# Performance work log

Hardware: AMD Instinct MI355X
Metric: run time of the kernel (lower is better)

Reference implementation:

```python
import jax, jax.numpy as jnp
import numpy as np

B, H, W, C = 16, 64, 64, 256
HEADS, WS, SHIFTS, QD = 8, 8, (0, 4), 512
N = WS * WS
HD = C // HEADS
MLP_H = 4 * C
DEPTH = 2
EPS = 1e-5


def _rel_pos_index():
    coords = np.stack(np.meshgrid(np.arange(WS), np.arange(WS), indexing='ij'))  # [2,ws,ws]
    flat = coords.reshape(2, -1)
    rel = (flat[:, :, None] - flat[:, None, :]).transpose(1, 2, 0)  # [N,N,2]
    rel[..., 0] += WS - 1
    rel[..., 1] += WS - 1
    rel[..., 0] *= 2 * WS - 1
    return jnp.asarray(rel.sum(-1))  # [N,N] int


def _shift_mask(shift):
    img = np.zeros((H, W))
    cnt = 0
    for hs in (slice(0, -WS), slice(-WS, -shift), slice(-shift, None)):
        for ws_ in (slice(0, -WS), slice(-WS, -shift), slice(-shift, None)):
            img[hs, ws_] = cnt
            cnt += 1
    mw = img.reshape(H // WS, WS, W // WS, WS).transpose(0, 2, 1, 3).reshape(-1, N)  # [nW,N]
    am = mw[:, None, :] - mw[:, :, None]
    return jnp.asarray(np.where(am != 0, -100.0, 0.0).astype(np.float32))  # [nW,N,N]


RPI = _rel_pos_index()


def layernorm(x, g, b):
    mu = x.mean(-1, keepdims=True)
    var = ((x - mu) ** 2).mean(-1, keepdims=True)
    return (x - mu) * jax.lax.rsqrt(var + EPS) * g + b


def window_partition(x):  # [B,H,W,C] -> [B*nW, N, C]
    x = x.reshape(B, H // WS, WS, W // WS, WS, C)
    return x.transpose(0, 1, 3, 2, 4, 5).reshape(-1, N, C)


def window_reverse(w):  # [B*nW, N, C] -> [B,H,W,C]
    x = w.reshape(B, H // WS, W // WS, WS, WS, C)
    return x.transpose(0, 1, 3, 2, 4, 5).reshape(B, H, W, C)


def swin_block(x, shift, n1g, n1b, qkvw, qkvb, rpb, pw, pb, n2g, n2b, f1w, f1b, f2w, f2b):
    shortcut = x
    y = layernorm(x, n1g, n1b).reshape(B, H, W, C)
    if shift > 0:
        y = jnp.roll(y, (-shift, -shift), axis=(1, 2))
    xw = window_partition(y)                                      # [B_, N, C]
    qkv = (xw @ qkvw + qkvb).reshape(-1, N, 3, HEADS, HD)
    q, k, v = (qkv[:, :, i].transpose(0, 2, 1, 3) for i in range(3))  # [B_,h,N,hd]
    scores = jnp.einsum('bhnd,bhmd->bhnm', q * (HD ** -0.5), k)
    bias = rpb[RPI].transpose(2, 0, 1)                            # [h,N,N]
    scores = scores + bias[None]
    if shift > 0:
        mask = _shift_mask(shift)                                 # [nW,N,N]
        nW = mask.shape[0]
        scores = scores.reshape(B, nW, HEADS, N, N) + mask[None, :, None]
        scores = scores.reshape(-1, HEADS, N, N)
    attn = jax.nn.softmax(scores, axis=-1)
    out = jnp.einsum('bhnm,bhmd->bhnd', attn, v).transpose(0, 2, 1, 3).reshape(-1, N, C)
    out = out @ pw + pb
    y = window_reverse(out)
    if shift > 0:
        y = jnp.roll(y, (shift, shift), axis=(1, 2))
    x = shortcut + y.reshape(B, H * W, C)
    h = layernorm(x, n2g, n2b)
    h = jax.nn.gelu(h @ f1w + f1b, approximate=False) @ f2w + f2b
    return x + h


def cross_attn(x, cond, cng, cnb, inw, inb, outw, outb):
    xn = layernorm(x, cng, cnb)
    q = xn @ inw[:C].T + inb[:C]
    k = cond @ inw[C:2 * C].T + inb[C:2 * C]
    v = cond @ inw[2 * C:].T + inb[2 * C:]
    Tq, Tk = q.shape[1], k.shape[1]
    q = q.reshape(B, Tq, HEADS, HD).transpose(0, 2, 1, 3) * (HD ** -0.5)
    k = k.reshape(B, Tk, HEADS, HD).transpose(0, 2, 1, 3)
    v = v.reshape(B, Tk, HEADS, HD).transpose(0, 2, 1, 3)
    a = jax.nn.softmax(jnp.einsum('bhqd,bhkd->bhqk', q, k), axis=-1)
    o = jnp.einsum('bhqk,bhkd->bhqd', a, v).transpose(0, 2, 1, 3).reshape(B, Tq, C)
    return x + o @ outw.T + outb


def setup_inputs() -> dict:
    key = jax.random.key(0)
    ks = iter(jax.random.split(key, 40))
    s = 0.02
    d = {
        'x': jax.random.normal(next(ks), (B, H * W, C), jnp.float32),
        'emb': jax.random.normal(next(ks), (B, 1, QD), jnp.float32),
        'qenc_w': jax.random.normal(next(ks), (QD, C)) * s,
        'qenc_b': jnp.zeros((C,)),
        'n1_g': jnp.ones((DEPTH, C)), 'n1_b': jnp.zeros((DEPTH, C)),
        'qkv_w': jax.random.normal(next(ks), (DEPTH, C, 3 * C)) * s,
        'qkv_b': jnp.zeros((DEPTH, 3 * C)),
        'rpb': jax.random.normal(next(ks), (DEPTH, (2 * WS - 1) ** 2, HEADS)) * s,
        'proj_w': jax.random.normal(next(ks), (DEPTH, C, C)) * s,
        'proj_b': jnp.zeros((DEPTH, C)),
        'n2_g': jnp.ones((DEPTH, C)), 'n2_b': jnp.zeros((DEPTH, C)),
        'fc1_w': jax.random.normal(next(ks), (DEPTH, C, MLP_H)) * s,
        'fc1_b': jnp.zeros((DEPTH, MLP_H)),
        'fc2_w': jax.random.normal(next(ks), (DEPTH, MLP_H, C)) * s,
        'fc2_b': jnp.zeros((DEPTH, C)),
        'cn_g': jnp.ones((DEPTH, C)), 'cn_b': jnp.zeros((DEPTH, C)),
        'ca_in_w': jax.random.normal(next(ks), (DEPTH, 3 * C, C)) * s,
        'ca_in_b': jnp.zeros((DEPTH, 3 * C)),
        'ca_out_w': jax.random.normal(next(ks), (DEPTH, C, C)) * s,
        'ca_out_b': jnp.zeros((DEPTH, C)),
    }
    return d


def reference(x, emb, qenc_w, qenc_b, n1_g, n1_b, qkv_w, qkv_b, rpb, proj_w, proj_b,
              n2_g, n2_b, fc1_w, fc1_b, fc2_w, fc2_b, cn_g, cn_b,
              ca_in_w, ca_in_b, ca_out_w, ca_out_b):
    for d in range(DEPTH):
        x = swin_block(x, SHIFTS[d], n1_g[d], n1_b[d], qkv_w[d], qkv_b[d], rpb[d],
                       proj_w[d], proj_b[d], n2_g[d], n2_b[d],
                       fc1_w[d], fc1_b[d], fc2_w[d], fc2_b[d])
        cond = emb @ qenc_w + qenc_b  # recomputed per block as in original
        x = cross_attn(x, cond, cn_g[d], cn_b[d], ca_in_w[d], ca_in_b[d],
                       ca_out_w[d], ca_out_b[d])
    return x
```

## Files before the change

kernel.cpp:

```cpp
#include <hip/hip_runtime.h>


typedef unsigned short bfraw;
typedef short s16x8 __attribute__((ext_vector_type(8)));
typedef short s16x4 __attribute__((ext_vector_type(4)));
typedef float f32x4 __attribute__((ext_vector_type(4)));

#define DEV static __device__ __forceinline__

DEV float b2f(int u){
  union { unsigned int i; float f; } x;
  x.i = ((unsigned int)u & 0xffffu) << 16;
  return x.f;
}
DEV unsigned short f2bbits(float f){
  union { float f; unsigned int i; } x; x.f = f;
  unsigned int i = x.i;
  unsigned int lsb = (i >> 16) & 1u;
  i += 0x7fffu + lsb;
  return (unsigned short)(i >> 16);
}

#define GLOAD_LDS16(g, l) __builtin_amdgcn_global_load_lds(                      \
    (const __attribute__((address_space(1))) void*)(g),                          \
    (__attribute__((address_space(3))) void*)(l), 16, 0, 0)

__global__ void k_copy(const float* __restrict__ xin, float* __restrict__ xfp){
  size_t i = ((size_t)blockIdx.x * 256 + threadIdx.x) * 4;
  *(float4*)(xfp + i) = *(const float4*)(xin + i);
}

__global__ void k_tr(const float* __restrict__ in, bfraw* __restrict__ out, int K, int N){
  int idx = blockIdx.x * 256 + threadIdx.x;
  if (idx >= K * N) return;
  int n = idx / K, k = idx - n * K;
  out[idx] = f2bbits(in[(size_t)k * N + n]);
}

__global__ __launch_bounds__(256) void k_ln(
    const float* __restrict__ x, const float* __restrict__ g,
    const float* __restrict__ b, bfraw* __restrict__ y)
{
  const int lane = threadIdx.x & 63, wv = threadIdx.x >> 6;
  const size_t row = (size_t)blockIdx.x * 4 + wv;
  const float4 v = *(const float4*)(x + row * 256 + lane * 4);
  float s  = v.x + v.y + v.z + v.w;
  float s2 = v.x*v.x + v.y*v.y + v.z*v.z + v.w*v.w;
#pragma unroll
  for (int off = 32; off; off >>= 1){
    s  += __shfl_xor(s,  off);
    s2 += __shfl_xor(s2, off);
  }
  float mu  = s * (1.f/256.f);
  float var = s2 * (1.f/256.f) - mu * mu;
  float rs  = rsqrtf(var + 1e-5f);
  const float4 gv = *(const float4*)(g + lane * 4);
  const float4 bv = *(const float4*)(b + lane * 4);
  s16x4 o;
  o[0] = (short)f2bbits((v.x - mu) * rs * gv.x + bv.x);
  o[1] = (short)f2bbits((v.y - mu) * rs * gv.y + bv.y);
  o[2] = (short)f2bbits((v.z - mu) * rs * gv.z + bv.z);
  o[3] = (short)f2bbits((v.w - mu) * rs * gv.w + bv.w);
  *(s16x4*)(y + row * 256 + lane * 4) = o;
}

template<int EPI>
__global__ __launch_bounds__(256, 2) void k_gemm(
    const bfraw* __restrict__ A, const bfraw* __restrict__ Bt,
    const float* __restrict__ bias,
    bfraw* __restrict__ Cout, int ldc,
    float* __restrict__ xfp,
    const float* __restrict__ addv,
    int M, int N, int K, int shift)
{
  constexpr int BK = 64;
  __shared__ __align__(16) bfraw sA[128 * BK];
  __shared__ __align__(16) bfraw sB[128 * BK];
  const int tid = threadIdx.x, lane = tid & 63, w = tid >> 6;
  const int nbm = M >> 7;
  const int tm = blockIdx.x % nbm, tn = blockIdx.x / nbm;
  const int m0 = tm << 7, n0 = tn << 7;
  const int wm = w & 1, wn = w >> 1;
  f32x4 acc[4][4] = {};

  const int srow = (w << 5) + (lane >> 3);
  const int scol = (lane & 7) << 3;
  const bfraw* gA = A  + (size_t)(m0 + srow) * K + scol;
  const bfraw* gB = Bt + (size_t)(n0 + srow) * K + scol;

  for (int kt = 0; kt < K; kt += BK){
    __syncthreads();
#pragma unroll
    for (int i = 0; i < 4; ++i){
      GLOAD_LDS16(gA + (size_t)(i * 8) * K + kt, &sA[(w * 4 + i) * 512]);
      GLOAD_LDS16(gB + (size_t)(i * 8) * K + kt, &sB[(w * 4 + i) * 512]);
    }
    __syncthreads();
#pragma unroll
    for (int ks = 0; ks < 2; ++ks){
      const int ko = ks * 32 + ((lane >> 4) << 3);
      s16x8 af[4], bfr[4];
#pragma unroll
      for (int i = 0; i < 4; ++i){
        af[i]  = *(const s16x8*)&sA[((wm << 6) + (i << 4) + (lane & 15)) * BK + ko];
        bfr[i] = *(const s16x8*)&sB[((wn << 6) + (i << 4) + (lane & 15)) * BK + ko];
      }
#pragma unroll
      for (int mi = 0; mi < 4; ++mi)
#pragma unroll
        for (int ni = 0; ni < 4; ++ni)
          acc[mi][ni] = __builtin_amdgcn_mfma_f32_16x16x32_bf16(
              af[mi], bfr[ni], acc[mi][ni], 0, 0, 0);
    }
  }

  const int cl = lane & 15;
  float bv[4];
#pragma unroll
  for (int ni = 0; ni < 4; ++ni) bv[ni] = bias[n0 + (wn << 6) + (ni << 4) + cl];

#pragma unroll
  for (int mi = 0; mi < 4; ++mi){
#pragma unroll
    for (int j = 0; j < 4; ++j){
      const int r = m0 + (wm << 6) + (mi << 4) + ((lane >> 4) << 2) + j;
      size_t rowoff;
      if constexpr (EPI == 2){
        int b_ = r >> 12, rem = r & 4095;
        int wi = rem >> 6, n_ = rem & 63;
        int gi = ((wi >> 3) * 8 + (n_ >> 3) + shift) & 63;
        int gj = ((wi & 7) * 8 + (n_ & 7) + shift) & 63;
        rowoff = ((size_t)b_ << 12) + gi * 64 + gj;
      } else {
        rowoff = (size_t)r;
      }
#pragma unroll
      for (int ni = 0; ni < 4; ++ni){
        float val = acc[mi][ni][j] + bv[ni];
        const int c = n0 + (wn << 6) + (ni << 4) + cl;
        if constexpr (EPI == 0){
          Cout[(size_t)r * ldc + c] = f2bbits(val);
        } else if constexpr (EPI == 1){
          val = 0.5f * val * (1.0f + erff(val * 0.70710678118654752f));
          Cout[(size_t)r * ldc + c] = f2bbits(val);
        } else if constexpr (EPI == 2){
          xfp[rowoff * 256 + c] += val;
        } else {
          size_t o = rowoff * 256 + c;
          xfp[o] = xfp[o] + val + addv[(size_t)(r >> 12) * 256 + c];
        }
      }
    }
  }
}

__global__ __launch_bounds__(64) void k_bias(const float* __restrict__ rpb,
                                             float* __restrict__ biasPk)
{
  const int blk = blockIdx.x;
  const int d = blk >> 5, cls = (blk >> 3) & 3, h = blk & 7;
  const int l = threadIdx.x, lo16 = l & 15, hg = l >> 4;
  const float* rp = rpb + (size_t)d * 225 * 8;
  float* ob = biasPk + (((size_t)d * 4 + cls) * 8 + h) * 4096;
#pragma unroll
  for (int mi = 0; mi < 4; ++mi)
#pragma unroll
    for (int ni = 0; ni < 4; ++ni)
#pragma unroll
      for (int j = 0; j < 4; ++j){
        int k = 16 * mi + 4 * hg + j, q = 16 * ni + lo16;
        int qr = q >> 3, qc = q & 7, kr = k >> 3, kc = k & 7;
        float v = rp[((qr - kr + 7) * 15 + (qc - kc + 7)) * 8 + h];
        if (d == 1){
          int lq = ((cls >> 1) ? (qr < 4 ? 1 : 2) : 0) * 3 + ((cls & 1) ? (qc < 4 ? 1 : 2) : 0);
          int lk = ((cls >> 1) ? (kr < 4 ? 1 : 2) : 0) * 3 + ((cls & 1) ? (kc < 4 ? 1 : 2) : 0);
          if (lq != lk) v -= 100.f;
        }
        ob[(mi * 4 + ni) * 256 + l * 4 + j] = v;
      }
}

__global__ __launch_bounds__(64) void k_attn(
    const bfraw* __restrict__ qkv, const float* __restrict__ biasPk,
    bfraw* __restrict__ aout, int shift)
{
  __shared__ __align__(16) bfraw sV[64 * 32];
  __shared__ __align__(16) bfraw sP[64 * 64];
  const int win = blockIdx.x >> 3, h = blockIdx.x & 7;
  const int b = win >> 6, wr = (win >> 3) & 7, wc = win & 7;
  const int l = threadIdx.x, lo16 = l & 15, hg = l >> 4;

  auto grow_of = [&](int n) -> size_t {
    int gi = (wr * 8 + (n >> 3) + shift) & 63;
    int gj = (wc * 8 + (n & 7) + shift) & 63;
    return ((size_t)b << 12) + gi * 64 + gj;
  };

  s16x8 vreg[4];
#pragma unroll
  for (int i = 0; i < 4; ++i){
    int row = i * 16 + (l >> 2);
    vreg[i] = *(const s16x8*)(qkv + grow_of(row) * 768 + 512 + h * 32 + (l & 3) * 8);
  }
#pragma unroll
  for (int i = 0; i < 4; ++i)
    *(s16x8*)&sV[i * 512 + l * 8] = vreg[i];

  s16x8 aK[4], bQ[4];
#pragma unroll
  for (int t = 0; t < 4; ++t){
    const bfraw* base = qkv + grow_of(16 * t + lo16) * 768 + h * 32 + hg * 8;
    bQ[t] = *(const s16x8*)base;
    aK[t] = *(const s16x8*)(base + 256);
  }

  f32x4 acc[4][4] = {};
#pragma unroll
  for (int mi = 0; mi < 4; ++mi)
#pragma unroll
    for (int ni = 0; ni < 4; ++ni)
      acc[mi][ni] = __builtin_amdgcn_mfma_f32_16x16x32_bf16(aK[mi], bQ[ni], acc[mi][ni], 0, 0, 0);

  const int cls = ((wr == 7) ? 2 : 0) | ((wc == 7) ? 1 : 0);
  const float* bb = biasPk + ((size_t)(cls * 8 + h)) * 4096;
#pragma unroll
  for (int mi = 0; mi < 4; ++mi)
#pragma unroll
    for (int ni = 0; ni < 4; ++ni){
      f32x4 bv4 = *(const f32x4*)(bb + (mi * 4 + ni) * 256 + l * 4);
      acc[mi][ni] = acc[mi][ni] * 0.17677669529663689f + bv4;
    }

#pragma unroll
  for (int ni = 0; ni < 4; ++ni){
    float m = acc[0][ni][0];
#pragma unroll
    for (int mi = 0; mi < 4; ++mi)
#pragma unroll
      for (int j = 0; j < 4; ++j) m = fmaxf(m, acc[mi][ni][j]);
    m = fmaxf(m, __shfl_xor(m, 16));
    m = fmaxf(m, __shfl_xor(m, 32));
    float s = 0.f;
#pragma unroll
    for (int mi = 0; mi < 4; ++mi)
#pragma unroll
      for (int j = 0; j < 4; ++j){
        float e = __expf(acc[mi][ni][j] - m);
        acc[mi][ni][j] = e; s += e;
      }
    s += __shfl_xor(s, 16);
    s += __shfl_xor(s, 32);
    float inv = 1.f / s;
#pragma unroll
    for (int mi = 0; mi < 4; ++mi)
#pragma unroll
      for (int j = 0; j < 4; ++j) acc[mi][ni][j] *= inv;
  }

#pragma unroll
  for (int mi = 0; mi < 4; ++mi)
#pragma unroll
    for (int ni = 0; ni < 4; ++ni){
      unsigned int w0, w1;
      asm("v_cvt_pk_bf16_f32 %0, %1, %2" : "=v"(w0) : "v"(acc[mi][ni][0]), "v"(acc[mi][ni][1]));
      asm("v_cvt_pk_bf16_f32 %0, %1, %2" : "=v"(w1) : "v"(acc[mi][ni][2]), "v"(acc[mi][ni][3]));
      int q = 16 * ni + lo16;
      int ad = (q * 128 + (16 * mi + 4 * hg) * 2) ^ ((q & 7) << 4);
      *(uint2*)((char*)sP + ad) = make_uint2(w0, w1);
    }

  asm volatile("s_waitcnt lgkmcnt(0)" ::: "memory");
  __builtin_amdgcn_sched_barrier(0);

  f32x4 opv[4][2] = {};
#pragma unroll
  for (int kt = 0; kt < 2; ++kt){
    s16x8 ap[4];
#pragma unroll
    for (int qi = 0; qi < 4; ++qi){
      int q = 16 * qi + lo16;
      int ad = (q * 128 + (kt * 32 + hg * 8) * 2) ^ ((q & 7) << 4);
      ap[qi] = *(const s16x8*)((const char*)sP + ad);
    }
    s16x8 vb[2];
#pragma unroll
    for (int nt = 0; nt < 2; ++nt)
#pragma unroll
      for (int e = 0; e < 8; ++e)
        vb[nt][e] = (short)sV[(kt * 32 + hg * 8 + e) * 32 + nt * 16 + lo16];
#pragma unroll
    for (int qi = 0; qi < 4; ++qi)
#pragma unroll
      for (int nt = 0; nt < 2; ++nt)
        opv[qi][nt] = __builtin_amdgcn_mfma_f32_16x16x32_bf16(ap[qi], vb[nt], opv[qi][nt], 0, 0, 0);
  }

  bfraw* ob = aout + ((size_t)win * 64) * 256 + h * 32 + lo16;
#pragma unroll
  for (int qi = 0; qi < 4; ++qi)
#pragma unroll
    for (int nt = 0; nt < 2; ++nt)
#pragma unroll
      for (int j = 0; j < 4; ++j)
        ob[(size_t)(16 * qi + 4 * hg + j) * 256 + nt * 16] = f2bbits(opv[qi][nt][j]);
}

__global__ __launch_bounds__(256) void k_addvec(
    const float* __restrict__ emb, const float* __restrict__ qw, const float* __restrict__ qb,
    const float* __restrict__ inw, const float* __restrict__ inb,
    const float* __restrict__ outw, const float* __restrict__ outb,
    float* __restrict__ addv)
{
  const int d = blockIdx.x >> 4, b = blockIdx.x & 15;
  const int j = threadIdx.x;
  __shared__ float sc[256], sv[256];
  float a = qb[j];
  for (int k = 0; k < 512; ++k) a = fmaf(emb[b * 512 + k], qw[k * 256 + j], a);
  sc[j] = a; __syncthreads();
  float v = inb[d * 768 + 512 + j];
  const float* wrp = inw + (size_t)d * 768 * 256 + (size_t)(512 + j) * 256;
  for (int k = 0; k < 256; ++k) v = fmaf(sc[k], wrp[k], v);
  sv[j] = v; __syncthreads();
  float o = outb[d * 256 + j];
  const float* wop = outw + (size_t)d * 65536 + (size_t)j * 256;
  for (int k = 0; k < 256; ++k) o = fmaf(sv[k], wop[k], o);
  addv[(size_t)(d * 16 + b) * 256 + j] = o;
}

extern "C" void kernel_launch(void* const* d_in, const int* in_sizes, int n_in,
                              void* d_out, int out_size, void* d_ws, size_t ws_size,
                              hipStream_t stream)
{
  (void)in_sizes; (void)n_in; (void)out_size; (void)ws_size;
  const float* x_in     = (const float*)d_in[0];
  const float* emb      = (const float*)d_in[1];
  const float* qenc_w   = (const float*)d_in[2];
  const float* qenc_b   = (const float*)d_in[3];
  const float* n1_g     = (const float*)d_in[4];
  const float* n1_b     = (const float*)d_in[5];
  const float* qkv_w    = (const float*)d_in[6];
  const float* qkv_b    = (const float*)d_in[7];
  const float* rpb      = (const float*)d_in[8];
  const float* proj_w   = (const float*)d_in[9];
  const float* proj_b   = (const float*)d_in[10];
  const float* n2_g     = (const float*)d_in[11];
  const float* n2_b     = (const float*)d_in[12];
  const float* fc1_w    = (const float*)d_in[13];
  const float* fc1_b    = (const float*)d_in[14];
  const float* fc2_w    = (const float*)d_in[15];
  const float* fc2_b    = (const float*)d_in[16];
  const float* ca_in_w  = (const float*)d_in[19];
  const float* ca_in_b  = (const float*)d_in[20];
  const float* ca_out_w = (const float*)d_in[21];
  const float* ca_out_b = (const float*)d_in[22];

  float* xfp  = (float*)d_out;
  char* ws = (char*)d_ws;
  bfraw* ybuf = (bfraw*)ws;
  bfraw* qkvb = (bfraw*)(ws + ((size_t)32 << 20));
  bfraw* wT   = (bfraw*)(ws + ((size_t)160 << 20));
  float* biasPk = (float*)(ws + ((size_t)166 << 20));

  bfraw *qkvT[2], *projT[2], *fc1T[2], *fc2T[2];
  size_t off = 0;
  for (int d = 0; d < 2; ++d){ qkvT[d] = wT + off; off += 768 * 256; }
  for (int d = 0; d < 2; ++d){ projT[d] = wT + off; off += 256 * 256; }
  for (int d = 0; d < 2; ++d){ fc1T[d] = wT + off; off += 1024 * 256; }
  for (int d = 0; d < 2; ++d){ fc2T[d] = wT + off; off += 256 * 1024; }
  float* addv = (float*)(wT + ((off + 1) & ~(size_t)1));

  for (int d = 0; d < 2; ++d){
    k_tr<<<(256 * 768  + 255) / 256, 256, 0, stream>>>(qkv_w  + (size_t)d * 256 * 768,  qkvT[d], 256, 768);
    k_tr<<<(256 * 256  + 255) / 256, 256, 0, stream>>>(proj_w + (size_t)d * 256 * 256,  projT[d], 256, 256);
    k_tr<<<(256 * 1024 + 255) / 256, 256, 0, stream>>>(fc1_w  + (size_t)d * 256 * 1024, fc1T[d], 256, 1024);
    k_tr<<<(1024 * 256 + 255) / 256, 256, 0, stream>>>(fc2_w  + (size_t)d * 1024 * 256, fc2T[d], 1024, 256);
  }
  k_bias<<<64, 64, 0, stream>>>(rpb, biasPk);
  k_addvec<<<32, 256, 0, stream>>>(emb, qenc_w, qenc_b, ca_in_w, ca_in_b, ca_out_w, ca_out_b, addv);
  k_copy<<<16384, 256, 0, stream>>>(x_in, xfp);

  for (int d = 0; d < 2; ++d){
    const int shift = d ? 4 : 0;
    k_ln<<<16384, 256, 0, stream>>>(xfp, n1_g + d * 256, n1_b + d * 256, ybuf);
    k_gemm<0><<<512 * 6, 256, 0, stream>>>(ybuf, qkvT[d], qkv_b + d * 768, qkvb, 768,
                                           nullptr, nullptr, 65536, 768, 256, 0);
    k_attn<<<8192, 64, 0, stream>>>(qkvb, biasPk + (size_t)d * 4 * 8 * 4096, ybuf, shift);
    k_gemm<2><<<512 * 2, 256, 0, stream>>>(ybuf, projT[d], proj_b + d * 256, nullptr, 0,
                                           xfp, nullptr, 65536, 256, 256, shift);
    k_ln<<<16384, 256, 0, stream>>>(xfp, n2_g + d * 256, n2_b + d * 256, ybuf);
    k_gemm<1><<<512 * 8, 256, 0, stream>>>(ybuf, fc1T[d], fc1_b + d * 1024, qkvb, 1024,
                                           nullptr, nullptr, 65536, 1024, 256, 0);
    k_gemm<3><<<512 * 2, 256, 0, stream>>>(qkvb, fc2T[d], fc2_b + d * 256, nullptr, 0,
                                           xfp, addv + (size_t)d * 16 * 256,
                                           65536, 256, 1024, 0);
  }
}
```

Before: 763.9 us.

## Swizzle GEMM LDS, remap workgroups, vectorize epilogues, tanh GELU, drop input copy

Several GEMM changes land together. LDS tiles get an XOR swizzle to avoid bank conflicts, workgroups are remapped across XCDs, and the MFMA operands are swapped so each lane holds four contiguous output columns. That lets the epilogues use vector loads and stores and fold in bias, residual and addv. The erf GELU is replaced by a tanh/sigmoid approximation, which changes numerics slightly, and the initial input copy kernel is removed by having the first residual add read x_in directly.

```diff
diff --git a/kernel.cpp b/kernel.cpp
--- a/kernel.cpp
+++ b/kernel.cpp
@@ -20,15 +20,15 @@
   i += 0x7fffu + lsb;
   return (unsigned short)(i >> 16);
 }
+DEV float gelu_tanh(float x){
+  float t2 = 1.5957691216057308f * fmaf(0.044715f * x * x, x, x);
+  float e = __expf(-t2);
+  return x * __builtin_amdgcn_rcpf(1.f + e);
+}
 
 #define GLOAD_LDS16(g, l) __builtin_amdgcn_global_load_lds(                      \
     (const __attribute__((address_space(1))) void*)(g),                          \
     (__attribute__((address_space(3))) void*)(l), 16, 0, 0)
-
-__global__ void k_copy(const float* __restrict__ xin, float* __restrict__ xfp){
-  size_t i = ((size_t)blockIdx.x * 256 + threadIdx.x) * 4;
-  *(float4*)(xfp + i) = *(const float4*)(xin + i);
-}
 
 __global__ void k_tr(const float* __restrict__ in, bfraw* __restrict__ out, int K, int N){
   int idx = blockIdx.x * 256 + threadIdx.x;
@@ -69,7 +69,7 @@
     const bfraw* __restrict__ A, const bfraw* __restrict__ Bt,
     const float* __restrict__ bias,
     bfraw* __restrict__ Cout, int ldc,
-    float* __restrict__ xfp,
+    float* __restrict__ xfp, const float* __restrict__ xin,
     const float* __restrict__ addv,
     int M, int N, int K, int shift)
 {
@@ -77,14 +77,19 @@
   __shared__ __align__(16) bfraw sA[128 * BK];
   __shared__ __align__(16) bfraw sB[128 * BK];
   const int tid = threadIdx.x, lane = tid & 63, w = tid >> 6;
-  const int nbm = M >> 7;
-  const int tm = blockIdx.x % nbm, tn = blockIdx.x / nbm;
+  const int lo16 = lane & 15, hg = lane >> 4;
+  const int nbm = M >> 7, nbn = N >> 7;
+  const int nwg = nbm * nbn;
+  const int bid = blockIdx.x;
+  const int wgid = (bid & 7) * (nwg >> 3) + (bid >> 3);
+  const int tn = wgid % nbn, tm = wgid / nbn;
   const int m0 = tm << 7, n0 = tn << 7;
   const int wm = w & 1, wn = w >> 1;
   f32x4 acc[4][4] = {};
 
   const int srow = (w << 5) + (lane >> 3);
-  const int scol = (lane & 7) << 3;
+  const int scol = (((lane & 7) ^ (lane >> 3)) << 3);
+  const int ksw  = (lane & 7) << 3;
   const bfraw* gA = A  + (size_t)(m0 + srow) * K + scol;
   const bfraw* gB = Bt + (size_t)(n0 + srow) * K + scol;
 
@@ -98,57 +103,65 @@
     __syncthreads();
 #pragma unroll
     for (int ks = 0; ks < 2; ++ks){
-      const int ko = ks * 32 + ((lane >> 4) << 3);
+      const int ko = (ks * 32 + (hg << 3)) ^ ksw;
       s16x8 af[4], bfr[4];
 #pragma unroll
       for (int i = 0; i < 4; ++i){
-        af[i]  = *(const s16x8*)&sA[((wm << 6) + (i << 4) + (lane & 15)) * BK + ko];
-        bfr[i] = *(const s16x8*)&sB[((wn << 6) + (i << 4) + (lane & 15)) * BK + ko];
-      }
-#pragma unroll
-      for (int mi = 0; mi < 4; ++mi)
-#pragma unroll
-        for (int ni = 0; ni < 4; ++ni)
-          acc[mi][ni] = __builtin_amdgcn_mfma_f32_16x16x32_bf16(
-              af[mi], bfr[ni], acc[mi][ni], 0, 0, 0);
-    }
-  }
-
-  const int cl = lane & 15;
-  float bv[4];
-#pragma unroll
-  for (int ni = 0; ni < 4; ++ni) bv[ni] = bias[n0 + (wn << 6) + (ni << 4) + cl];
+        af[i]  = *(const s16x8*)&sA[((wm << 6) + (i << 4) + lo16) * BK + ko];
+        bfr[i] = *(const s16x8*)&sB[((wn << 6) + (i << 4) + lo16) * BK + ko];
+      }
+#pragma unroll
+      for (int ni = 0; ni < 4; ++ni)
+#pragma unroll
+        for (int mi = 0; mi < 4; ++mi)
+          acc[ni][mi] = __builtin_amdgcn_mfma_f32_16x16x32_bf16(
+              bfr[ni], af[mi], acc[ni][mi], 0, 0, 0);
+    }
+  }
+
+  const int cb = n0 + (wn << 6) + 4 * hg;
+  f32x4 bv4[4];
+#pragma unroll
+  for (int ni = 0; ni < 4; ++ni) bv4[ni] = *(const f32x4*)(bias + cb + ni * 16);
 
 #pragma unroll
   for (int mi = 0; mi < 4; ++mi){
-#pragma unroll
-    for (int j = 0; j < 4; ++j){
-      const int r = m0 + (wm << 6) + (mi << 4) + ((lane >> 4) << 2) + j;
-      size_t rowoff;
-      if constexpr (EPI == 2){
-        int b_ = r >> 12, rem = r & 4095;
-        int wi = rem >> 6, n_ = rem & 63;
-        int gi = ((wi >> 3) * 8 + (n_ >> 3) + shift) & 63;
-        int gj = ((wi & 7) * 8 + (n_ & 7) + shift) & 63;
-        rowoff = ((size_t)b_ << 12) + gi * 64 + gj;
-      } else {
-        rowoff = (size_t)r;
-      }
+    const int r = m0 + (wm << 6) + (mi << 4) + lo16;
+    if constexpr (EPI == 0 || EPI == 1){
+      bfraw* crow = Cout + (size_t)r * ldc + cb;
 #pragma unroll
       for (int ni = 0; ni < 4; ++ni){
-        float val = acc[mi][ni][j] + bv[ni];
-        const int c = n0 + (wn << 6) + (ni << 4) + cl;
-        if constexpr (EPI == 0){
-          Cout[(size_t)r * ldc + c] = f2bbits(val);
-        } else if constexpr (EPI == 1){
-          val = 0.5f * val * (1.0f + erff(val * 0.70710678118654752f));
-          Cout[(size_t)r * ldc + c] = f2bbits(val);
-        } else if constexpr (EPI == 2){
-          xfp[rowoff * 256 + c] += val;
-        } else {
-          size_t o = rowoff * 256 + c;
-          xfp[o] = xfp[o] + val + addv[(size_t)(r >> 12) * 256 + c];
+        f32x4 v = acc[ni][mi] + bv4[ni];
+        s16x4 o;
+#pragma unroll
+        for (int j = 0; j < 4; ++j){
+          float val = v[j];
+          if constexpr (EPI == 1) val = gelu_tanh(val);
+          o[j] = (short)f2bbits(val);
         }
+        *(s16x4*)(crow + ni * 16) = o;
+      }
+    } else if constexpr (EPI == 2){
+      int b_ = r >> 12, rem = r & 4095;
+      int wi = rem >> 6, n_ = rem & 63;
+      int gi = ((wi >> 3) * 8 + (n_ >> 3) + shift) & 63;
+      int gj = ((wi & 7) * 8 + (n_ & 7) + shift) & 63;
+      size_t rowoff = ((size_t)b_ << 12) + gi * 64 + gj;
+      const float* xi = xin + rowoff * 256 + cb;
+      float*       xo = xfp + rowoff * 256 + cb;
+#pragma unroll
+      for (int ni = 0; ni < 4; ++ni){
+        f32x4 v = acc[ni][mi] + bv4[ni] + *(const f32x4*)(xi + ni * 16);
+        *(f32x4*)(xo + ni * 16) = v;
+      }
+    } else {
+      const float* av = addv + (size_t)(r >> 12) * 256 + cb;
+      float* xo = xfp + (size_t)r * 256 + cb;
+#pragma unroll
+      for (int ni = 0; ni < 4; ++ni){
+        f32x4 v = acc[ni][mi] + bv4[ni] + *(const f32x4*)(xo + ni * 16)
+                + *(const f32x4*)(av + ni * 16);
+        *(f32x4*)(xo + ni * 16) = v;
       }
     }
   }
@@ -377,21 +390,21 @@
   }
   k_bias<<<64, 64, 0, stream>>>(rpb, biasPk);
   k_addvec<<<32, 256, 0, stream>>>(emb, qenc_w, qenc_b, ca_in_w, ca_in_b, ca_out_w, ca_out_b, addv);
-  k_copy<<<16384, 256, 0, stream>>>(x_in, xfp);
 
   for (int d = 0; d < 2; ++d){
     const int shift = d ? 4 : 0;
-    k_ln<<<16384, 256, 0, stream>>>(xfp, n1_g + d * 256, n1_b + d * 256, ybuf);
+    const float* resid_in = d ? (const float*)xfp : x_in;
+    k_ln<<<16384, 256, 0, stream>>>(resid_in, n1_g + d * 256, n1_b + d * 256, ybuf);
     k_gemm<0><<<512 * 6, 256, 0, stream>>>(ybuf, qkvT[d], qkv_b + d * 768, qkvb, 768,
-                                           nullptr, nullptr, 65536, 768, 256, 0);
+                                           nullptr, nullptr, nullptr, 65536, 768, 256, 0);
     k_attn<<<8192, 64, 0, stream>>>(qkvb, biasPk + (size_t)d * 4 * 8 * 4096, ybuf, shift);
     k_gemm<2><<<512 * 2, 256, 0, stream>>>(ybuf, projT[d], proj_b + d * 256, nullptr, 0,
-                                           xfp, nullptr, 65536, 256, 256, shift);
+                                           xfp, resid_in, nullptr, 65536, 256, 256, shift);
     k_ln<<<16384, 256, 0, stream>>>(xfp, n2_g + d * 256, n2_b + d * 256, ybuf);
     k_gemm<1><<<512 * 8, 256, 0, stream>>>(ybuf, fc1T[d], fc1_b + d * 1024, qkvb, 1024,
-                                           nullptr, nullptr, 65536, 1024, 256, 0);
+                                           nullptr, nullptr, nullptr, 65536, 1024, 256, 0);
     k_gemm<3><<<512 * 2, 256, 0, stream>>>(qkvb, fc2T[d], fc2_b + d * 256, nullptr, 0,
-                                           xfp, addv + (size_t)d * 16 * 256,
+                                           xfp, nullptr, addv + (size_t)d * 16 * 256,
                                            65536, 256, 1024, 0);
   }
 }
```

After: 686.2 us. -10.2%, faster.
